# Performance work log

Hardware: AMD Instinct MI355X
Metric: run time of the kernel (lower is better)

## Reference

```python
import jax, jax.numpy as jnp
import numpy as np

B, S, D = 4, 1024, 4096
HQ, HKV, HD = 32, 8, 128
N_REP = HQ // HKV


def _rope(x, cos, sin):
    # x: [b, s, h, hd]; cos/sin: [s, hd//2]; pairs are (x[..., 2i], x[..., 2i+1])
    xr = x[..., 0::2]
    xi = x[..., 1::2]
    c = cos[None, :, None, :]
    s = sin[None, :, None, :]
    out_r = xr * c - xi * s
    out_i = xr * s + xi * c
    return jnp.stack([out_r, out_i], axis=-1).reshape(x.shape)


def setup_inputs() -> dict:
    key = jax.random.key(0)
    ks = jax.random.split(key, 6)
    x = jax.random.normal(ks[0], (B, S, D), dtype=jnp.float32)
    wq = jax.random.normal(ks[1], (HQ * HD, D), dtype=jnp.float32) * 0.02
    wk = jax.random.normal(ks[2], (HKV * HD, D), dtype=jnp.float32) * 0.02
    wv = jax.random.normal(ks[3], (HKV * HD, D), dtype=jnp.float32) * 0.02
    wo = jax.random.normal(ks[4], (D, HQ * HD), dtype=jnp.float32) * 0.02
    # standard rotary frequencies, theta=10000
    inv_freq = 1.0 / (10000.0 ** (np.arange(0, HD, 2, dtype=np.float32) / HD))
    angles = np.outer(np.arange(S, dtype=np.float32), inv_freq)  # [S, HD//2]
    freqs_cos = jnp.asarray(np.cos(angles), dtype=jnp.float32)
    freqs_sin = jnp.asarray(np.sin(angles), dtype=jnp.float32)
    cache_k = jnp.zeros((B, S, HKV, HD), dtype=jnp.float32)
    cache_v = jnp.zeros((B, S, HKV, HD), dtype=jnp.float32)
    return {"x": x, "wq": wq, "wk": wk, "wv": wv, "wo": wo,
            "freqs_cos": freqs_cos, "freqs_sin": freqs_sin,
            "cache_k": cache_k, "cache_v": cache_v, "start_pos": 0}


def reference(x, wq, wk, wv, wo, freqs_cos, freqs_sin, cache_k, cache_v, start_pos):
    b, s, _ = x.shape
    xq = jnp.einsum('bsd,od->bso', x, wq).reshape(b, s, HQ, HD)
    xk = jnp.einsum('bsd,od->bso', x, wk).reshape(b, s, HKV, HD)
    xv = jnp.einsum('bsd,od->bso', x, wv).reshape(b, s, HKV, HD)
    xq = _rope(xq, freqs_cos, freqs_sin)
    xk = _rope(xk, freqs_cos, freqs_sin)
    # KV-cache append (intended semantics: store keys/values)
    cache_k = jax.lax.dynamic_update_slice(cache_k, xk, (0, start_pos, 0, 0))
    cache_v = jax.lax.dynamic_update_slice(cache_v, xv, (0, start_pos, 0, 0))
    keys = cache_k[:, :start_pos + s]      # [b, kv, HKV, HD]
    values = cache_v[:, :start_pos + s]
    # GQA repeat_kv -> [b, kv, HQ, HD]
    keys = jnp.repeat(keys, N_REP, axis=2)
    values = jnp.repeat(values, N_REP, axis=2)
    scores = jnp.einsum('bqhd,bkhd->bhqk', xq, keys) / jnp.sqrt(jnp.float32(HD))
    probs = jax.nn.softmax(scores.astype(jnp.float32), axis=-1).astype(xq.dtype)
    out = jnp.einsum('bhqk,bkhd->bqhd', probs, values).reshape(b, s, HQ * HD)
    return jnp.einsum('bso,do->bsd', out, wo)
```

## Files before the change

### kernel.cpp

```cpp
#include <hip/hip_runtime.h>

typedef __bf16 bf16_t;
typedef __bf16 bf16x8 __attribute__((ext_vector_type(8)));
typedef __bf16 bf16x4 __attribute__((ext_vector_type(4)));
typedef float  f32x4  __attribute__((ext_vector_type(4)));
typedef short  s16x4  __attribute__((ext_vector_type(4)));

#define SEQ    1024
#define DMODEL 4096
#define NHQ    32
#define NHKV   8
#define HDIM   128

#define GLOAD_LDS16(g, l)                                                  \
    __builtin_amdgcn_global_load_lds(                                      \
        (const __attribute__((address_space(1))) unsigned int*)(g),        \
        (__attribute__((address_space(3))) unsigned int*)(l), 16, 0, 0)

__global__ __launch_bounds__(256)
void f2b(const float* __restrict__ in, bf16_t* __restrict__ out, int n8)
{
    int i = blockIdx.x * 256 + threadIdx.x;
    if (i >= n8) return;
    const float4* p = (const float4*)in + 2 * (size_t)i;
    float4 a = p[0], b = p[1];
    bf16x8 o;
    o[0] = (bf16_t)a.x; o[1] = (bf16_t)a.y; o[2] = (bf16_t)a.z; o[3] = (bf16_t)a.w;
    o[4] = (bf16_t)b.x; o[5] = (bf16_t)b.y; o[6] = (bf16_t)b.z; o[7] = (bf16_t)b.w;
    *((bf16x8*)out + i) = o;
}

#define MFMA_(a, b, c) __builtin_amdgcn_mfma_f32_16x16x32_bf16(a, b, c, 0, 0, 0)
#define BAR    __builtin_amdgcn_s_barrier()
#define SCB    __builtin_amdgcn_sched_barrier(0)
#define PRIO1  __builtin_amdgcn_s_setprio(1)
#define PRIO0  __builtin_amdgcn_s_setprio(0)
#define WLG0   do { asm volatile("s_waitcnt lgkmcnt(0)" ::: "memory"); SCB; } while (0)
#define WLG8   do { asm volatile("s_waitcnt lgkmcnt(8)" ::: "memory"); SCB; } while (0)
#define WVM4   do { asm volatile("s_waitcnt vmcnt(4)" ::: "memory"); SCB; } while (0)

#define SA(bufo, half, ktb)  do {                                          \
    const char* g_ = ((half) ? aS1 : aS0) + (ktb);                         \
    GLOAD_LDS16(g_,      sd + (bufo) + (half) * 8192);                     \
    GLOAD_LDS16(g_ + 64, sd + (bufo) + (half) * 8192 + 16384);             \
} while (0)
#define SB(bufo, half, ktb)  do {                                          \
    const char* g_ = ((half) ? bS1 : bS0) + (ktb);                         \
    GLOAD_LDS16(g_,      sd + (bufo) + 32768 + (half) * 8192);             \
    GLOAD_LDS16(g_ + 64, sd + (bufo) + 32768 + (half) * 8192 + 16384);     \
} while (0)
#define LDA(bufo, mh) do { _Pragma("unroll")                               \
    for (int j = 0; j < 4; ++j) {                                          \
        afq[j][0] = *(const bf16x8*)(lds + (bufo) + aRow + (mh)*4096 + j*1024);         \
        afq[j][1] = *(const bf16x8*)(lds + (bufo) + aRow + (mh)*4096 + j*1024 + 16384); \
    } } while (0)
#define LDB(bufo, nh, dst) do { _Pragma("unroll")                          \
    for (int n2 = 0; n2 < 2; ++n2) {                                       \
        dst[n2][0] = *(const bf16x8*)(lds + (bufo) + bRow + (nh)*2048 + n2*1024);         \
        dst[n2][1] = *(const bf16x8*)(lds + (bufo) + bRow + (nh)*2048 + n2*1024 + 16384); \
    } } while (0)
#define MMQ(mlo, bfx, nlo) do { _Pragma("unroll")                          \
    for (int j = 0; j < 4; ++j) {                                          \
        acc[(mlo)+j][(nlo)  ] = MFMA_(afq[j][0], bfx[0][0], acc[(mlo)+j][(nlo)  ]); \
        acc[(mlo)+j][(nlo)  ] = MFMA_(afq[j][1], bfx[0][1], acc[(mlo)+j][(nlo)  ]); \
        acc[(mlo)+j][(nlo)+1] = MFMA_(afq[j][0], bfx[1][0], acc[(mlo)+j][(nlo)+1]); \
        acc[(mlo)+j][(nlo)+1] = MFMA_(afq[j][1], bfx[1][1], acc[(mlo)+j][(nlo)+1]); \
    } } while (0)

template<bool OUT_F32>
__global__ __launch_bounds__(512, 2)
void gemm256(const bf16_t* __restrict__ A, const bf16_t* __restrict__ B,
             void* __restrict__ Cv, int M, int N, int K, int nbn)
{
    __shared__ __align__(16) char lds[131072];

    const int nwg = gridDim.x;
    const int bid0 = blockIdx.x;
    const int bid = (bid0 & 7) * (nwg >> 3) + (bid0 >> 3);
    const int bm = bid / nbn, bn = bid % nbn;
    const int t = threadIdx.x;
    const int lane = t & 63, wid = t >> 6;
    const int wm = wid >> 2, wn = wid & 3;
    const int l15 = lane & 15, lg = lane >> 4;
    const int m0 = bm * 256, n0 = bn * 256;

    const int Krb = K * 2;
    const int srow = t >> 2;
    const int schunk = (((t & 3) ^ ((t >> 3) & 3)) << 4);
    const char* aS0 = (const char*)A + (size_t)(m0 + srow) * Krb + schunk;
    const char* aS1 = (const char*)A + (size_t)(m0 + 128 + srow) * Krb + schunk;
    const char* bS0 = (const char*)B + (size_t)(n0 + srow) * Krb + schunk;
    const char* bS1 = (const char*)B + (size_t)(n0 + 128 + srow) * Krb + schunk;
    char* sd = lds + t * 16;

    const int rchunk = ((lg ^ ((l15 >> 1) & 3)) << 4);
    const int aRow = (wm * 128 + l15) * 64 + rchunk;
    const int bRow = 32768 + (wn * 64 + l15) * 64 + rchunk;

    const int NT = K >> 6;
    f32x4 acc[8][4] = {};
    bf16x8 afq[4][2], bf0[2][2], bf1[2][2];

    SA(0, 0, 0); SA(0, 1, 0); SB(0, 0, 0); SB(0, 1, 0);
    SB(65536, 0, 128); SB(65536, 1, 128);
    WVM4;
    BAR;

    for (int T = 0; T < NT; T += 2) {
        const int k1 = (T + 1) * 128;
        const int k2 = (T + 2 < NT) ? (T + 2) * 128 : 0;
        const int k3 = (T + 3 < NT) ? (T + 3) * 128 : 0;
        LDA(0, 0); LDB(0, 0, bf0); SA(65536, 0, k1); WLG8; BAR; WLG0;
        PRIO1; MMQ(0, bf0, 0); PRIO0; BAR;
        LDB(0, 1, bf1); SA(65536, 1, k1); BAR; WLG0;
        PRIO1; MMQ(0, bf1, 2); PRIO0; BAR;
        LDA(0, 1); SB(0, 0, k2); BAR; WLG0;
        PRIO1; MMQ(4, bf1, 2); PRIO0; BAR;
        SB(0, 1, k2); BAR;
        PRIO1; MMQ(4, bf0, 0); PRIO0; WVM4; BAR;
        LDA(65536, 0); LDB(65536, 0, bf0); SA(0, 0, k2); WLG8; BAR; WLG0;
        PRIO1; MMQ(0, bf0, 0); PRIO0; BAR;
        LDB(65536, 1, bf1); SA(0, 1, k2); BAR; WLG0;
        PRIO1; MMQ(0, bf1, 2); PRIO0; BAR;
        LDA(65536, 1); SB(65536, 0, k3); BAR; WLG0;
        PRIO1; MMQ(4, bf1, 2); PRIO0; BAR;
        SB(65536, 1, k3); BAR;
        PRIO1; MMQ(4, bf0, 0); PRIO0; WVM4; BAR;
    }

    #pragma unroll
    for (int m = 0; m < 8; ++m) {
        int row0 = m0 + wm * 128 + m * 16 + lg * 4;
        #pragma unroll
        for (int n = 0; n < 4; ++n) {
            int col = n0 + wn * 64 + n * 16 + l15;
            #pragma unroll
            for (int i = 0; i < 4; ++i) {
                if constexpr (OUT_F32)
                    ((float*)Cv)[(size_t)(row0 + i) * N + col] = acc[m][n][i];
                else
                    ((bf16_t*)Cv)[(size_t)(row0 + i) * N + col] = (bf16_t)acc[m][n][i];
            }
        }
    }
}

template<int MODE>
__global__ __launch_bounds__(256, 4)
void gemm_bt(const bf16_t* __restrict__ A, const bf16_t* __restrict__ B,
             void* __restrict__ Cv, bf16_t* __restrict__ Vt,
             int M, int N, int K, int nbn)
{
    __shared__ __align__(16) bf16_t lA[128 * 32];
    __shared__ __align__(16) bf16_t lB[128 * 32];

    const int nwg = gridDim.x;
    const int bid0 = blockIdx.x;
    const int bid = (bid0 & 7) * (nwg >> 3) + (bid0 >> 3);
    const int bm = bid / nbn, bn = bid % nbn;
    const int t = threadIdx.x;
    const int lane = t & 63, wid = t >> 6;
    const int wrow = (wid >> 1) * 64, wcol = (wid & 1) * 64;
    const int l15 = lane & 15, lg = lane >> 4;
    const int m0 = bm * 128, n0 = bn * 128;

    const int r0 = t >> 2, pos0 = (t & 3) * 8;
    const int r1 = r0 + 64;

    const bf16_t* Ar0 = A + (size_t)(m0 + r0) * K + pos0;
    const bf16_t* Ar1 = A + (size_t)(m0 + r1) * K + pos0;
    const bf16_t* Br0 = B + (size_t)(n0 + r0) * K + pos0;
    const bf16_t* Br1 = B + (size_t)(n0 + r1) * K + pos0;

    f32x4 acc[4][4] = {};

    for (int k0 = 0; k0 < K; k0 += 32) {
        __syncthreads();
        GLOAD_LDS16(Ar0 + k0, lA + t * 8);
        GLOAD_LDS16(Ar1 + k0, lA + (t + 256) * 8);
        GLOAD_LDS16(Br0 + k0, lB + t * 8);
        GLOAD_LDS16(Br1 + k0, lB + (t + 256) * 8);
        __syncthreads();

        bf16x8 af[4], bfr[4];
        #pragma unroll
        for (int m = 0; m < 4; ++m)
            af[m] = *(const bf16x8*)(lA + (wrow + m * 16 + l15) * 32 + lg * 8);
        #pragma unroll
        for (int n = 0; n < 4; ++n)
            bfr[n] = *(const bf16x8*)(lB + (wcol + n * 16 + l15) * 32 + lg * 8);
        #pragma unroll
        for (int m = 0; m < 4; ++m)
            #pragma unroll
            for (int n = 0; n < 4; ++n)
                acc[m][n] = __builtin_amdgcn_mfma_f32_16x16x32_bf16(
                    af[m], bfr[n], acc[m][n], 0, 0, 0);
    }

    #pragma unroll
    for (int m = 0; m < 4; ++m) {
        #pragma unroll
        for (int n = 0; n < 4; ++n) {
            int col  = n0 + wcol + n * 16 + l15;
            int row0 = m0 + wrow + m * 16 + lg * 4;
            if constexpr (MODE == 0) {
                #pragma unroll
                for (int i = 0; i < 4; ++i)
                    ((bf16_t*)Cv)[(size_t)(row0 + i) * N + col] = (bf16_t)acc[m][n][i];
            } else if constexpr (MODE == 1) {
                #pragma unroll
                for (int i = 0; i < 4; ++i)
                    ((float*)Cv)[(size_t)(row0 + i) * N + col] = acc[m][n][i];
            } else {
                if (col < 1024) {
                    #pragma unroll
                    for (int i = 0; i < 4; ++i)
                        ((bf16_t*)Cv)[(size_t)(row0 + i) * 1024 + col] = (bf16_t)acc[m][n][i];
                } else {
                    bf16x4 pk;
                    #pragma unroll
                    for (int i = 0; i < 4; ++i) pk[i] = (bf16_t)acc[m][n][i];
                    *(bf16x4*)(Vt + (size_t)(col - 1024) * 4096 + row0) = pk;
                }
            }
        }
    }
}

__global__ __launch_bounds__(256)
void rope_kernel(bf16_t* __restrict__ X, const float* __restrict__ fc,
                 const float* __restrict__ fs, int nheads, int rowstride,
                 float oscale)
{
    int idx = blockIdx.x * 256 + threadIdx.x;
    int j4 = idx & 15;
    int rest = idx >> 4;
    int h = rest % nheads;
    int tok = rest / nheads;
    int s = tok & (SEQ - 1);
    bf16_t* p = X + (size_t)tok * rowstride + h * HDIM + j4 * 8;
    bf16x8 v = *(const bf16x8*)p;
    float4 c  = *(const float4*)(fc + s * 64 + j4 * 4);
    float4 sn = *(const float4*)(fs + s * 64 + j4 * 4);
    c.x *= oscale; c.y *= oscale; c.z *= oscale; c.w *= oscale;
    sn.x *= oscale; sn.y *= oscale; sn.z *= oscale; sn.w *= oscale;
    bf16x8 o;
    o[0] = (bf16_t)((float)v[0] * c.x - (float)v[1] * sn.x);
    o[1] = (bf16_t)((float)v[0] * sn.x + (float)v[1] * c.x);
    o[2] = (bf16_t)((float)v[2] * c.y - (float)v[3] * sn.y);
    o[3] = (bf16_t)((float)v[2] * sn.y + (float)v[3] * c.y);
    o[4] = (bf16_t)((float)v[4] * c.z - (float)v[5] * sn.z);
    o[5] = (bf16_t)((float)v[4] * sn.z + (float)v[5] * c.z);
    o[6] = (bf16_t)((float)v[6] * c.w - (float)v[7] * sn.w);
    o[7] = (bf16_t)((float)v[6] * sn.w + (float)v[7] * c.w);
    *(bf16x8*)p = o;
}

__global__ __launch_bounds__(512, 2)
void attn_kernel(const bf16_t* __restrict__ Q, const bf16_t* __restrict__ Kg,
                 const bf16_t* __restrict__ Vtg, bf16_t* __restrict__ O)
{
    __shared__ __align__(16) char klds[2][64 * 256];
    __shared__ __align__(16) char vlds[2][128 * 128];

    const int nwg = gridDim.x;
    const int bid0 = blockIdx.x;
    const int blk = (bid0 & 7) * (nwg >> 3) + (bid0 >> 3);
    const int qt = blk & 7;
    const int bh = blk >> 3;
    const int b = bh >> 5, h = bh & 31, kv = h >> 2;
    const int t = threadIdx.x, lane = t & 63, wid = t >> 6;
    const int l15 = lane & 15, lg = lane >> 4;
    const int swzk = (l15 & 7) << 4;

    const float L2E = 1.4426950408889634f;

    const int qrow = qt * 128 + wid * 16 + l15;
    const size_t qbase = (size_t)(b * SEQ + qrow) * DMODEL + h * HDIM;
    bf16x8 qf[4];
    #pragma unroll
    for (int dc = 0; dc < 4; ++dc)
        qf[dc] = *(const bf16x8*)(Q + qbase + dc * 32 + lg * 8);

    const char* kgb = (const char*)Kg + ((size_t)(b * SEQ) * 1024 + kv * HDIM) * 2;
    const char* vgb = (const char*)Vtg + ((size_t)(kv * HDIM) * 4096 + b * SEQ) * 2;

    const int ck0 = t, ck1 = t + 512;
    const int kr0 = ck0 >> 4, kf0 = kr0 * 2048 + ((((ck0 & 15) << 4)) ^ ((kr0 & 7) << 4));
    const int kr1 = ck1 >> 4, kf1 = kr1 * 2048 + ((((ck1 & 15) << 4)) ^ ((kr1 & 7) << 4));
    const int vd0 = ck0 >> 3, vf0 = vd0 * 8192 + ((((ck0 & 7) << 4)) ^ ((vd0 & 7) << 4));
    const int vd1 = ck1 >> 3, vf1 = vd1 * 8192 + ((((ck1 & 7) << 4)) ^ ((vd1 & 7) << 4));

    f32x4 o[8] = {};
    float mrun = -3.0e38f, lrun = 0.f;

#define STAGE_KV(kt_, bi_) do {                                            \
    GLOAD_LDS16(kgb + (size_t)(kt_) * 131072 + kf0, klds[bi_] + ck0 * 16); \
    GLOAD_LDS16(kgb + (size_t)(kt_) * 131072 + kf1, klds[bi_] + ck1 * 16); \
    GLOAD_LDS16(vgb + (kt_) * 128 + vf0, vlds[bi_] + ck0 * 16);            \
    GLOAD_LDS16(vgb + (kt_) * 128 + vf1, vlds[bi_] + ck1 * 16);            \
} while (0)

    STAGE_KV(0, 0);
    __syncthreads();

    for (int kt = 0; kt < 16; ++kt) {
        const int cur = kt & 1;
        const int knx = (kt + 1 < 16) ? kt + 1 : 15;
        STAGE_KV(knx, cur ^ 1);

        f32x4 sacc[4] = {};
        #pragma unroll
        for (int kb = 0; kb < 4; ++kb) {
            const char* krow = klds[cur] + (kb * 16 + l15) * 256;
            #pragma unroll
            for (int dc = 0; dc < 4; ++dc) {
                bf16x8 kf = *(const bf16x8*)(krow + ((dc * 64 + lg * 16) ^ swzk));
                sacc[kb] = __builtin_amdgcn_mfma_f32_16x16x32_bf16(
                    kf, qf[dc], sacc[kb], 0, 0, 0);
            }
        }

        float sv[16];
        float mt = -3.0e38f;
        #pragma unroll
        for (int kb = 0; kb < 4; ++kb)
            #pragma unroll
            for (int i = 0; i < 4; ++i) {
                float s = sacc[kb][i];
                sv[kb * 4 + i] = s;
                mt = fmaxf(mt, s);
            }
        mt = fmaxf(mt, __shfl_xor(mt, 16));
        mt = fmaxf(mt, __shfl_xor(mt, 32));
        float mnew = fmaxf(mrun, mt);
        float alpha = exp2f((mrun - mnew) * L2E);

        float ts = 0.f;
        s16x4 pf[4];
        #pragma unroll
        for (int kb = 0; kb < 4; ++kb)
            #pragma unroll
            for (int i = 0; i < 4; ++i) {
                float p = exp2f((sv[kb * 4 + i] - mnew) * L2E);
                ts += p;
                pf[kb][i] = (short)__builtin_bit_cast(unsigned short, (bf16_t)p);
            }
        ts += __shfl_xor(ts, 16);
        ts += __shfl_xor(ts, 32);
        lrun = lrun * alpha + ts;
        mrun = mnew;

        #pragma unroll
        for (int i = 0; i < 4; ++i) {
            float ai = __shfl(alpha, lg * 4 + i);
            #pragma unroll
            for (int db = 0; db < 8; ++db) o[db][i] *= ai;
        }

        #pragma unroll
        for (int kb = 0; kb < 4; ++kb)
            #pragma unroll
            for (int db = 0; db < 8; ++db) {
                int d = l15 + 16 * db;
                const char* va = vlds[cur] + d * 128 + ((kb * 32 + lg * 8) ^ swzk);
                s16x4 vf = *(const s16x4*)va;
                o[db] = __builtin_amdgcn_mfma_f32_16x16x16bf16_1k(
                    pf[kb], vf, o[db], 0, 0, 0);
            }

        __syncthreads();
    }
#undef STAGE_KV

    #pragma unroll
    for (int i = 0; i < 4; ++i) {
        float li = __shfl(lrun, lg * 4 + i);
        float inv = 1.0f / li;
        int row = b * SEQ + qt * 128 + wid * 16 + lg * 4 + i;
        #pragma unroll
        for (int db = 0; db < 8; ++db) {
            int col = h * HDIM + l15 + 16 * db;
            O[(size_t)row * DMODEL + col] = (bf16_t)(o[db][i] * inv);
        }
    }
}

extern "C" void kernel_launch(void* const* d_in, const int* in_sizes, int n_in,
                              void* d_out, int out_size, void* d_ws, size_t ws_size,
                              hipStream_t stream)
{
    const float* x  = (const float*)d_in[0];
    const float* wq = (const float*)d_in[1];
    const float* wk = (const float*)d_in[2];
    const float* wv = (const float*)d_in[3];
    const float* wo = (const float*)d_in[4];
    const float* fc = (const float*)d_in[5];
    const float* fs = (const float*)d_in[6];

    const size_t T = (size_t)4096;
    bf16_t* Qw   = (bf16_t*)d_ws;
    bf16_t* Kw2  = Qw   + T * 4096;
    bf16_t* Vt   = Kw2  + T * 1024;
    bf16_t* AO   = Vt   + T * 1024;
    bf16_t* xb   = AO   + T * 4096;
    bf16_t* wqb  = xb   + T * 4096;
    bf16_t* wkvb = wqb  + T * 4096;
    bf16_t* wob  = wkvb + T * 2048;

    f2b<<<8192, 256, 0, stream>>>(x,  xb,  4096 * 4096 / 8);
    f2b<<<8192, 256, 0, stream>>>(wq, wqb, 4096 * 4096 / 8);
    f2b<<<2048, 256, 0, stream>>>(wk, wkvb,                       1024 * 4096 / 8);
    f2b<<<2048, 256, 0, stream>>>(wv, wkvb + (size_t)1024 * 4096, 1024 * 4096 / 8);
    f2b<<<8192, 256, 0, stream>>>(wo, wob, 4096 * 4096 / 8);

    gemm256<false><<<256, 512, 0, stream>>>(xb, wqb, Qw, 4096, 4096, 4096, 16);
    gemm_bt<2><<<512, 256, 0, stream>>>(xb, wkvb, Kw2, Vt, 4096, 2048, 4096, 16);

    rope_kernel<<<8192, 256, 0, stream>>>(Qw,  fc, fs, NHQ,  4096,
                                          0.08838834764831845f);
    rope_kernel<<<2048, 256, 0, stream>>>(Kw2, fc, fs, NHKV, 1024, 1.0f);

    attn_kernel<<<1024, 512, 0, stream>>>(Qw, Kw2, Vt, AO);

    gemm256<true><<<256, 512, 0, stream>>>(AO, wob, d_out, 4096, 4096, 4096, 16);
}
```

Baseline: 519.3 us.

## Use 16x16x32 MFMA for PV via permuted K rows and lane shuffles

```diff
diff --git a/kernel.cpp b/kernel.cpp
--- a/kernel.cpp
+++ b/kernel.cpp
@@ -4,7 +4,7 @@
 typedef __bf16 bf16x8 __attribute__((ext_vector_type(8)));
 typedef __bf16 bf16x4 __attribute__((ext_vector_type(4)));
 typedef float  f32x4  __attribute__((ext_vector_type(4)));
-typedef short  s16x4  __attribute__((ext_vector_type(4)));
+typedef unsigned u32x4 __attribute__((ext_vector_type(4)));
 
 #define SEQ    1024
 #define DMODEL 4096
@@ -273,8 +273,6 @@
     const int l15 = lane & 15, lg = lane >> 4;
     const int swzk = (l15 & 7) << 4;
 
-    const float L2E = 1.4426950408889634f;
-
     const int qrow = qt * 128 + wid * 16 + l15;
     const size_t qbase = (size_t)(b * SEQ + qrow) * DMODEL + h * HDIM;
     bf16x8 qf[4];
@@ -286,8 +284,13 @@
     const char* vgb = (const char*)Vtg + ((size_t)(kv * HDIM) * 4096 + b * SEQ) * 2;
 
     const int ck0 = t, ck1 = t + 512;
-    const int kr0 = ck0 >> 4, kf0 = kr0 * 2048 + ((((ck0 & 15) << 4)) ^ ((kr0 & 7) << 4));
-    const int kr1 = ck1 >> 4, kf1 = kr1 * 2048 + ((((ck1 & 15) << 4)) ^ ((kr1 & 7) << 4));
+    const int kr0 = ck0 >> 4, kr1 = ck1 >> 4;
+    const int kg0 = ((kr0 >> 5) << 5) + (((((kr0 & 15) >> 2) ^ ((kr0 >> 4) & 1)) << 3))
+                  + (((kr0 >> 4) & 1) << 2) + (kr0 & 3);
+    const int kg1 = ((kr1 >> 5) << 5) + (((((kr1 & 15) >> 2) ^ ((kr1 >> 4) & 1)) << 3))
+                  + (((kr1 >> 4) & 1) << 2) + (kr1 & 3);
+    const int kf0 = kg0 * 2048 + ((((ck0 & 15) << 4)) ^ ((kr0 & 7) << 4));
+    const int kf1 = kg1 * 2048 + ((((ck1 & 15) << 4)) ^ ((kr1 & 7) << 4));
     const int vd0 = ck0 >> 3, vf0 = vd0 * 8192 + ((((ck0 & 7) << 4)) ^ ((vd0 & 7) << 4));
     const int vd1 = ck1 >> 3, vf1 = vd1 * 8192 + ((((ck1 & 7) << 4)) ^ ((vd1 & 7) << 4));
 
@@ -321,31 +324,29 @@
             }
         }
 
-        float sv[16];
         float mt = -3.0e38f;
         #pragma unroll
         for (int kb = 0; kb < 4; ++kb)
             #pragma unroll
-            for (int i = 0; i < 4; ++i) {
-                float s = sacc[kb][i];
-                sv[kb * 4 + i] = s;
-                mt = fmaxf(mt, s);
-            }
+            for (int i = 0; i < 4; ++i)
+                mt = fmaxf(mt, sacc[kb][i]);
         mt = fmaxf(mt, __shfl_xor(mt, 16));
         mt = fmaxf(mt, __shfl_xor(mt, 32));
         float mnew = fmaxf(mrun, mt);
-        float alpha = exp2f((mrun - mnew) * L2E);
+        float alpha = exp2f(mrun - mnew);
 
         float ts = 0.f;
-        s16x4 pf[4];
-        #pragma unroll
-        for (int kb = 0; kb < 4; ++kb)
-            #pragma unroll
-            for (int i = 0; i < 4; ++i) {
-                float p = exp2f((sv[kb * 4 + i] - mnew) * L2E);
-                ts += p;
-                pf[kb][i] = (short)__builtin_bit_cast(unsigned short, (bf16_t)p);
-            }
+        unsigned qpk[4][2];
+        #pragma unroll
+        for (int kb = 0; kb < 4; ++kb) {
+            float p0 = exp2f(sacc[kb][0] - mnew);
+            float p1 = exp2f(sacc[kb][1] - mnew);
+            float p2 = exp2f(sacc[kb][2] - mnew);
+            float p3 = exp2f(sacc[kb][3] - mnew);
+            ts += (p0 + p1) + (p2 + p3);
+            asm("v_cvt_pk_bf16_f32 %0, %1, %2" : "=v"(qpk[kb][0]) : "v"(p0), "v"(p1));
+            asm("v_cvt_pk_bf16_f32 %0, %1, %2" : "=v"(qpk[kb][1]) : "v"(p2), "v"(p3));
+        }
         ts += __shfl_xor(ts, 16);
         ts += __shfl_xor(ts, 32);
         lrun = lrun * alpha + ts;
@@ -359,15 +360,21 @@
         }
 
         #pragma unroll
-        for (int kb = 0; kb < 4; ++kb)
+        for (int c = 0; c < 2; ++c) {
+            unsigned s0 = (unsigned)__shfl_xor((int)qpk[2 * c + 1][0], 16);
+            unsigned s1 = (unsigned)__shfl_xor((int)qpk[2 * c + 1][1], 16);
+            u32x4 w;
+            w[0] = qpk[2 * c][0]; w[1] = qpk[2 * c][1]; w[2] = s0; w[3] = s1;
+            bf16x8 a32 = __builtin_bit_cast(bf16x8, w);
             #pragma unroll
             for (int db = 0; db < 8; ++db) {
                 int d = l15 + 16 * db;
-                const char* va = vlds[cur] + d * 128 + ((kb * 32 + lg * 8) ^ swzk);
-                s16x4 vf = *(const s16x4*)va;
-                o[db] = __builtin_amdgcn_mfma_f32_16x16x16bf16_1k(
-                    pf[kb], vf, o[db], 0, 0, 0);
+                const char* va = vlds[cur] + d * 128 + ((c * 64 + lg * 16) ^ swzk);
+                bf16x8 vf = *(const bf16x8*)va;
+                o[db] = __builtin_amdgcn_mfma_f32_16x16x32_bf16(
+                    a32, vf, o[db], 0, 0, 0);
             }
+        }
 
         __syncthreads();
     }
@@ -418,7 +425,7 @@
     gemm_bt<2><<<512, 256, 0, stream>>>(xb, wkvb, Kw2, Vt, 4096, 2048, 4096, 16);
 
     rope_kernel<<<8192, 256, 0, stream>>>(Qw,  fc, fs, NHQ,  4096,
-                                          0.08838834764831845f);
+                                          0.08838834764831845f * 1.4426950408889634f);
     rope_kernel<<<2048, 256, 0, stream>>>(Kw2, fc, fs, NHKV, 1024, 1.0f);
 
     attn_kernel<<<1024, 512, 0, stream>>>(Qw, Kw2, Vt, AO);
```

Result: faster. 499.1 us (-3.9%).
